# Kernel tuning notes

Hardware: AMD Instinct MI355X
Metric: run time of the kernel (lower is better)

Reference implementation:

```python
import jax, jax.numpy as jnp
import numpy as np

B, S, ENC = 64, 2048, 1024          # batch, encoder seq len, encoder feature dim
U, E_DIM, V_SZ = 512, 256, 50000    # dec_units, embedding_dim, vocab_size
IN_DIM = ENC + E_DIM                # LSTM input: [context ; token embedding]


def setup_inputs() -> dict:
    key = jax.random.key(0)
    ks = jax.random.split(key, 16)
    g = lambda k, shp, s=0.02: (jax.random.normal(k, shp, jnp.float32) * s)
    return {
        "x": jax.random.randint(ks[0], (B, 1), 0, V_SZ),
        "c_fwd": g(ks[1], (B, U), 0.1),
        "c_bwd": g(ks[2], (B, U), 0.1),
        "enc_output": jax.random.normal(ks[3], (B, S, ENC), jnp.float32),
        "emb": g(ks[4], (V_SZ, E_DIM)),
        "W1_w": g(ks[5], (ENC, U)), "W1_b": jnp.zeros((U,), jnp.float32),
        "W2_w": g(ks[6], (U, U)),   "W2_b": jnp.zeros((U,), jnp.float32),
        "W3_w": g(ks[7], (U, U)),   "W3_b": jnp.zeros((U,), jnp.float32),
        "V_w": g(ks[8], (U, 1)),    "V_b": jnp.zeros((1,), jnp.float32),
        "Kf": g(ks[9], (IN_DIM, 4 * U)),  "bf": jnp.zeros((4 * U,), jnp.float32),
        "Kb": g(ks[10], (IN_DIM, 4 * U)), "bb": jnp.zeros((4 * U,), jnp.float32),
        "fc_w": g(ks[11], (2 * U, V_SZ)), "fc_b": jnp.zeros((V_SZ,), jnp.float32),
    }


def _lstm_step_zero_state(xin, K, b):
    # Keras LSTM single step from zero (h0, c0): recurrent term vanishes.
    # Gate order in Keras kernel: i, f, c(g), o.
    z = xin @ K + b
    i, f, g, o = jnp.split(z, 4, axis=-1)
    i, o = jax.nn.sigmoid(i), jax.nn.sigmoid(o)  # f gate multiplies c0=0
    c = i * jnp.tanh(g)
    h = o * jnp.tanh(c)
    return h, c


def reference(x, c_fwd, c_bwd, enc_output, emb,
              W1_w, W1_b, W2_w, W2_b, W3_w, W3_b, V_w, V_b,
              Kf, bf, Kb, bb, fc_w, fc_b):
    # Bahdanau additive attention: score [B, S, 1]
    hidden_proj = (c_fwd @ W2_w + W2_b + c_bwd @ W3_w + W3_b)[:, None, :]  # [B,1,U]
    score = jnp.tanh(enc_output @ W1_w + W1_b + hidden_proj) @ V_w + V_b
    attn = jax.nn.softmax(score, axis=1)                 # softmax over S
    ctx = jnp.sum(attn * enc_output, axis=1)             # [B, ENC]

    xe = emb[x[:, 0]]                                    # [B, E_DIM]
    xin = jnp.concatenate([ctx, xe], axis=-1)            # [B, ENC+E_DIM]

    # Bidirectional LSTM over a length-1 sequence from zero initial state:
    # both directions see the same single timestep with separate weights.
    hf, cf = _lstm_step_zero_state(xin, Kf, bf)
    hb, cb = _lstm_step_zero_state(xin, Kb, bb)

    out = jnp.concatenate([hf, hb], axis=-1)             # [B, 2U]
    logits = out @ fc_w + fc_b                           # [B, vocab]
    return logits, hf, cf, hb, cb
```

## Files before the change

### kernel.cpp

```cpp
#include <hip/hip_runtime.h>

using u16 = unsigned short;
typedef float f32x4 __attribute__((ext_vector_type(4)));
typedef __bf16 bf16x8 __attribute__((ext_vector_type(8)));
typedef u16 u16x8 __attribute__((ext_vector_type(8)));
typedef u16 u16x4 __attribute__((ext_vector_type(4)));

static constexpr int OF_HPB   = 262144;
static constexpr int OF_CTXP  = 294912;
static constexpr int OF_STATS = 2392064;
static constexpr int OF_XIN   = 2394112;
static constexpr int OF_ZPART = 2476032;
static constexpr size_t SCRATCH_FLOATS = 3000320;
static constexpr size_t SCRATCH_BYTES  = SCRATCH_FLOATS * 4ull;
static constexpr size_t OF_W2P_F       = 3000320;
static constexpr size_t W2P_U16        = 50176ull * 1024ull;
static constexpr size_t TOTAL_BYTES    = OF_W2P_F * 4ull + W2P_U16 * 2ull;

#define FENCE()  asm volatile("" ::: "memory")
#define VMCNT6() asm volatile("s_waitcnt vmcnt(6)" ::: "memory")
#define VMCNT0() asm volatile("s_waitcnt vmcnt(0)" ::: "memory")
#define LGKM0()  asm volatile("s_waitcnt lgkmcnt(0)" ::: "memory")

__device__ __forceinline__ u16 f2bf(float f) {
  unsigned u = __float_as_uint(f);
  u += 0x7FFFu + ((u >> 16) & 1u);
  return (u16)(u >> 16);
}
__device__ __forceinline__ float bf2f(u16 u) {
  return __uint_as_float((unsigned)u << 16);
}
__device__ __forceinline__ float fast_tanh(float x) {
  x = fminf(fmaxf(x, -20.f), 20.f);
  float e = __expf(2.f * x);
  return (e - 1.f) / (e + 1.f);
}
__device__ __forceinline__ float fast_sig(float x) { return 1.f / (1.f + __expf(-x)); }

__device__ __forceinline__ void gll16(const u16* g, u16* l) {
  __builtin_amdgcn_global_load_lds(
      (const __attribute__((address_space(1))) unsigned int*)g,
      (__attribute__((address_space(3))) unsigned int*)l, 16, 0, 0);
}

__global__ void k_prep_w1(const float* __restrict__ W1w, u16* __restrict__ w1p) {
  __shared__ float tile[32][132];
  const int t = threadIdx.x;
  const int ks = blockIdx.x >> 2, u0 = (blockIdx.x & 3) * 128;
  {
    int kk = t >> 3, ui = (t & 7) * 16;
    const float* src = W1w + (size_t)(ks * 32 + kk) * 512 + u0 + ui;
    #pragma unroll
    for (int i = 0; i < 4; ++i)
      *(float4*)&tile[kk][ui + i * 4] = *(const float4*)(src + i * 4);
  }
  __syncthreads();
  {
    int u = t >> 1, kh = (t & 1) * 16;
    u16x8 p0, p1;
    #pragma unroll
    for (int i = 0; i < 8; ++i) {
      p0[i] = f2bf(tile[kh + i][u]);
      p1[i] = f2bf(tile[kh + 8 + i][u]);
    }
    u16* dst = w1p + ((size_t)ks * 512 + u0 + u) * 32 + kh;
    *(u16x8*)(dst)     = p0;
    *(u16x8*)(dst + 8) = p1;
  }
}

__global__ void k_prep_hp(const float* __restrict__ cf, const float* __restrict__ cb,
                          const float* __restrict__ W2w, const float* __restrict__ W2b,
                          const float* __restrict__ W3w, const float* __restrict__ W3b,
                          const float* __restrict__ W1b, float* __restrict__ hpb) {
  __shared__ float cfl[512], cbl[512];
  const int b = blockIdx.x, t = threadIdx.x;
  cfl[t] = cf[(size_t)b * 512 + t];       cfl[t + 256] = cf[(size_t)b * 512 + t + 256];
  cbl[t] = cb[(size_t)b * 512 + t];       cbl[t + 256] = cb[(size_t)b * 512 + t + 256];
  __syncthreads();
  const int u1 = t, u2 = t + 256;
  float a1 = W2b[u1] + W3b[u1] + W1b[u1];
  float a2 = W2b[u2] + W3b[u2] + W1b[u2];
  for (int k = 0; k < 512; ++k) {
    float c1 = cfl[k], c2 = cbl[k];
    const float* r2 = W2w + (size_t)k * 512;
    const float* r3 = W3w + (size_t)k * 512;
    a1 += c1 * r2[u1] + c2 * r3[u1];
    a2 += c1 * r2[u2] + c2 * r3[u2];
  }
  hpb[(size_t)b * 512 + u1] = a1;
  hpb[(size_t)b * 512 + u2] = a2;
}

__global__ void __launch_bounds__(256)
k_prep_fcw(const float* __restrict__ fcw, u16* __restrict__ w2p) {
  __shared__ float tl[32][260];
  const int t = threadIdx.x;
  const int jt = blockIdx.x >> 5, kt = blockIdx.x & 31;
  const int j0 = jt * 256, k0 = kt * 32;
  {
    const int kk = t >> 3, c0 = (t & 7) * 32;
    const float* src = fcw + (size_t)(k0 + kk) * 50000 + j0 + c0;
    #pragma unroll
    for (int i = 0; i < 8; ++i) {
      int j = j0 + c0 + i * 4;
      float4 v;
      if (j + 3 < 50000) {
        v = *(const float4*)(src + i * 4);
      } else {
        v.x = (j + 0 < 50000) ? src[i * 4 + 0] : 0.f;
        v.y = (j + 1 < 50000) ? src[i * 4 + 1] : 0.f;
        v.z = (j + 2 < 50000) ? src[i * 4 + 2] : 0.f;
        v.w = 0.f;
      }
      *(float4*)&tl[kk][c0 + i * 4] = v;
    }
  }
  __syncthreads();
  {
    u16* dst = w2p + ((size_t)kt * 50176 + j0 + t) * 32;
    #pragma unroll
    for (int q = 0; q < 4; ++q) {
      u16x8 p;
      #pragma unroll
      for (int m = 0; m < 8; ++m) p[m] = f2bf(tl[q * 8 + m][t]);
      *(u16x8*)(dst + q * 8) = p;
    }
  }
}

__global__ void __launch_bounds__(512, 4)
k_attn(const float* __restrict__ enc, const u16* __restrict__ w1p,
       const float* __restrict__ hpb, const float* __restrict__ Vw,
       const float* __restrict__ Vb, float* __restrict__ ctxp,
       float* __restrict__ stats) {
  __shared__ __align__(16) u16 smem[36864];

  const int t = threadIdx.x;
  const int bid = blockIdx.x;
  const int b = bid >> 5, tile = bid & 31;
  const size_t row0 = (size_t)b * 2048 + (size_t)tile * 64;

  const int l = t & 63, w = t >> 6;
  const int ln = l & 15, lg = l >> 4;

  const int s_im = t >> 7, s_ln = (t >> 3) & 15, s_lg = (t >> 1) & 3, s_h = t & 1;
  const float* a_src = enc + (row0 + s_im * 16 + s_ln) * 1024 + s_lg * 8 + s_h * 4;
  const int a_dst = (s_im * 64 + s_lg * 16 + s_ln) * 8 + s_h * 4;
  const u16* bsrc = w1p + (size_t)(w * 64 + ln) * 32 + lg * 8;
  u16* bdst = smem + w * 2048;

  f32x4 acc[4][4];
  #pragma unroll
  for (int im = 0; im < 4; ++im)
    #pragma unroll
    for (int nf = 0; nf < 4; ++nf) acc[im][nf] = f32x4{0.f, 0.f, 0.f, 0.f};

  float4 avH0, avH1, avH2;
  {
    float4 av0 = *(const float4*)(a_src);
    u16x4 aw;
    aw[0]=f2bf(av0.x); aw[1]=f2bf(av0.y); aw[2]=f2bf(av0.z); aw[3]=f2bf(av0.w);
    *(u16x4*)(smem + 32768 + a_dst) = aw;
    FENCE();
    avH0 = *(const float4*)(a_src + 32);
    avH1 = *(const float4*)(a_src + 64);
    FENCE();
    gll16(bsrc,        bdst);
    gll16(bsrc +  512, bdst +  512);
    gll16(bsrc + 1024, bdst + 1024);
    gll16(bsrc + 1536, bdst + 1536);
    FENCE();
    avH2 = *(const float4*)(a_src + 96);
    FENCE();
    LGKM0();
    __builtin_amdgcn_s_barrier();
  }

  #pragma unroll 4
  for (int ks = 0; ks < 28; ++ks) {
    const int cur = ks & 1;
    {
      u16* bd = bdst + ((cur ^ 1) << 14);
      const u16* bs = bsrc + (size_t)(ks + 1) * 16384;
      gll16(bs, bd);               gll16(bs +  512, bd +  512);
      gll16(bs + 1024, bd + 1024); gll16(bs + 1536, bd + 1536);
    }
    FENCE();
    float4 avIn = *(const float4*)(a_src + (ks + 4) * 32);
    FENCE();
    VMCNT6();
    const u16* Ac = smem + 32768 + (cur << 11);
    const u16* Bc = smem + (cur << 14) + w * 2048;
    bf16x8 afr[4], bfr[4];
    #pragma unroll
    for (int im = 0; im < 4; ++im) afr[im] = *(const bf16x8*)(Ac + im * 512 + l * 8);
    #pragma unroll
    for (int nf = 0; nf < 4; ++nf) bfr[nf] = *(const bf16x8*)(Bc + nf * 512 + l * 8);
    __builtin_amdgcn_s_setprio(1);
    #pragma unroll
    for (int im = 0; im < 4; ++im)
      #pragma unroll
      for (int nf = 0; nf < 4; ++nf)
        acc[im][nf] = __builtin_amdgcn_mfma_f32_16x16x32_bf16(afr[im], bfr[nf], acc[im][nf], 0, 0, 0);
    __builtin_amdgcn_s_setprio(0);
    {
      u16* An = smem + 32768 + ((cur ^ 1) << 11);
      u16x4 aw;
      aw[0]=f2bf(avH0.x); aw[1]=f2bf(avH0.y); aw[2]=f2bf(avH0.z); aw[3]=f2bf(avH0.w);
      *(u16x4*)(An + a_dst) = aw;
    }
    avH0 = avH1; avH1 = avH2; avH2 = avIn;
    LGKM0();
    __builtin_amdgcn_s_barrier();
  }

  for (int ks = 28; ks < 32; ++ks) {
    const int cur = ks & 1;
    if (ks < 31) {
      u16* bd = bdst + ((cur ^ 1) << 14);
      const u16* bs = bsrc + (size_t)(ks + 1) * 16384;
      gll16(bs, bd);               gll16(bs +  512, bd +  512);
      gll16(bs + 1024, bd + 1024); gll16(bs + 1536, bd + 1536);
    }
    VMCNT0();
    const u16* Ac = smem + 32768 + (cur << 11);
    const u16* Bc = smem + (cur << 14) + w * 2048;
    bf16x8 afr[4], bfr[4];
    #pragma unroll
    for (int im = 0; im < 4; ++im) afr[im] = *(const bf16x8*)(Ac + im * 512 + l * 8);
    #pragma unroll
    for (int nf = 0; nf < 4; ++nf) bfr[nf] = *(const bf16x8*)(Bc + nf * 512 + l * 8);
    #pragma unroll
    for (int im = 0; im < 4; ++im)
      #pragma unroll
      for (int nf = 0; nf < 4; ++nf)
        acc[im][nf] = __builtin_amdgcn_mfma_f32_16x16x32_bf16(afr[im], bfr[nf], acc[im][nf], 0, 0, 0);
    if (ks < 31) {
      u16* An = smem + 32768 + ((cur ^ 1) << 11);
      u16x4 aw;
      aw[0]=f2bf(avH0.x); aw[1]=f2bf(avH0.y); aw[2]=f2bf(avH0.z); aw[3]=f2bf(avH0.w);
      *(u16x4*)(An + a_dst) = aw;
      avH0 = avH1; avH1 = avH2;
    }
    LGKM0();
    __builtin_amdgcn_s_barrier();
  }

  float* fsm = (float*)smem;
  float* red = fsm;
  float* scv = fsm + 576;
  float* pcv = fsm + 640;

  float vw_l[4], hp_l[4];
  #pragma unroll
  for (int nf = 0; nf < 4; ++nf) {
    int col = w * 64 + nf * 16 + ln;
    vw_l[nf] = Vw[col];
    hp_l[nf] = hpb[(size_t)b * 512 + col];
  }
  #pragma unroll
  for (int im = 0; im < 4; ++im) {
    #pragma unroll
    for (int r = 0; r < 4; ++r) {
      float s = 0.f;
      #pragma unroll
      for (int nf = 0; nf < 4; ++nf)
        s += vw_l[nf] * fast_tanh(acc[im][nf][r] + hp_l[nf]);
      s += __shfl_xor(s, 1);
      s += __shfl_xor(s, 2);
      s += __shfl_xor(s, 4);
      s += __shfl_xor(s, 8);
      if (ln == 0) red[(im * 16 + lg * 4 + r) * 9 + w] = s;
    }
  }
  __syncthreads();
  if (t < 64) {
    float s = Vb[0];
    #pragma unroll
    for (int w2 = 0; w2 < 8; ++w2) s += red[t * 9 + w2];
    float e = __expf(s);
    scv[t] = e;
    float p = e;
    p += __shfl_xor(p, 1);  p += __shfl_xor(p, 2);  p += __shfl_xor(p, 4);
    p += __shfl_xor(p, 8);  p += __shfl_xor(p, 16); p += __shfl_xor(p, 32);
    if (t == 0) stats[bid] = p;
  }
  __syncthreads();

  {
    const int c4 = (t & 255) * 4;
    const int rh = t >> 8;
    const float* ep = enc + (row0 + rh * 32) * 1024 + c4;
    float ax = 0.f, ay = 0.f, az = 0.f, aw2 = 0.f;
    #pragma unroll 4
    for (int r = 0; r < 32; ++r) {
      float4 v = *(const float4*)(ep + (size_t)r * 1024);
      float s = scv[rh * 32 + r];
      ax += s * v.x; ay += s * v.y; az += s * v.z; aw2 += s * v.w;
    }
    if (t >= 256) {
      float4 st = {ax, ay, az, aw2};
      *(float4*)&pcv[c4] = st;
    }
    __syncthreads();
    if (t < 256) {
      float4 p2 = *(const float4*)&pcv[c4];
      float4 o = {ax + p2.x, ay + p2.y, az + p2.z, aw2 + p2.w};
      *(float4*)&ctxp[(size_t)bid * 1024 + c4] = o;
    }
  }
}

__global__ void k_attn_reduce(const float* __restrict__ ctxp, const float* __restrict__ stats,
                              const int* __restrict__ x, const float* __restrict__ emb,
                              float* __restrict__ xin) {
  __shared__ float ps[32];
  __shared__ float invs;
  const int b = blockIdx.x, t = threadIdx.x;
  if (t < 32) ps[t] = stats[b * 32 + t];
  __syncthreads();
  if (t == 0) {
    float s = 0.f;
    #pragma unroll
    for (int i = 0; i < 32; ++i) s += ps[i];
    invs = 1.f / s;
  }
  __syncthreads();
  const float inv = invs;
  #pragma unroll
  for (int i = 0; i < 4; ++i) {
    int c = t + i * 256;
    float a = 0.f;
    for (int chv = 0; chv < 32; ++chv)
      a += ctxp[((size_t)b * 32 + chv) * 1024 + c];
    xin[(size_t)b * 1280 + c] = a * inv;
  }
  xin[(size_t)b * 1280 + 1024 + t] = emb[(size_t)x[b] * 256 + t];
}

__global__ void k_lstm_gemm(const float* __restrict__ xin, const float* __restrict__ Kf,
                            const float* __restrict__ Kb, float* __restrict__ zpart) {
  __shared__ float xl[32][68];
  const int t = threadIdx.x;
  const int bid = blockIdx.x;
  const int dir = bid >> 7;
  const int jt  = (bid >> 1) & 63;
  const int ks  = bid & 1;
  const float* K = dir ? Kb : Kf;
  const int j  = jt * 32 + (t & 31);
  const int tb = t >> 5;
  const int brow = t >> 2, kq = (t & 3) * 8;
  float acc[8] = {0,0,0,0,0,0,0,0};
  for (int k0 = ks * 640; k0 < ks * 640 + 640; k0 += 32) {
    float4 x0 = *(const float4*)&xin[(size_t)brow * 1280 + k0 + kq];
    float4 x1 = *(const float4*)&xin[(size_t)brow * 1280 + k0 + kq + 4];
    __syncthreads();
    xl[kq+0][brow]=x0.x; xl[kq+1][brow]=x0.y; xl[kq+2][brow]=x0.z; xl[kq+3][brow]=x0.w;
    xl[kq+4][brow]=x1.x; xl[kq+5][brow]=x1.y; xl[kq+6][brow]=x1.z; xl[kq+7][brow]=x1.w;
    __syncthreads();
    const float* Kp = K + (size_t)k0 * 2048 + j;
    #pragma unroll 8
    for (int kk = 0; kk < 32; ++kk) {
      float wv = Kp[(size_t)kk * 2048];
      float4 v0 = *(const float4*)&xl[kk][tb * 8];
      float4 v1 = *(const float4*)&xl[kk][tb * 8 + 4];
      acc[0] += v0.x * wv; acc[1] += v0.y * wv; acc[2] += v0.z * wv; acc[3] += v0.w * wv;
      acc[4] += v1.x * wv; acc[5] += v1.y * wv; acc[6] += v1.z * wv; acc[7] += v1.w * wv;
    }
  }
  float* zp = zpart + ((size_t)dir * 2 + ks) * 64 * 2048;
  #pragma unroll
  for (int i = 0; i < 8; ++i)
    zp[(size_t)(tb * 8 + i) * 2048 + j] = acc[i];
}

__global__ void k_gates(const float* __restrict__ zpart, const float* __restrict__ bfv,
                        const float* __restrict__ bbv, float* __restrict__ dout) {
  const int dir = blockIdx.x >> 6, b = blockIdx.x & 63, u = threadIdx.x;
  const float* bias = dir ? bbv : bfv;
  const float* z0 = zpart + ((size_t)dir * 2 + 0) * 131072 + (size_t)b * 2048;
  const float* z1 = zpart + ((size_t)dir * 2 + 1) * 131072 + (size_t)b * 2048;
  float zi = z0[u]        + z1[u]        + bias[u];
  float zg = z0[1024 + u] + z1[1024 + u] + bias[1024 + u];
  float zo = z0[1536 + u] + z1[1536 + u] + bias[1536 + u];
  float c = fast_sig(zi) * fast_tanh(zg);
  float h = fast_sig(zo) * fast_tanh(c);
  size_t base = 3200000u + (size_t)dir * 65536u;
  dout[base + (size_t)b * 512 + u] = h;
  dout[base + 32768u + (size_t)b * 512 + u] = c;
}

__global__ void __launch_bounds__(256)
k_fc_mfma(const float* __restrict__ hbase, const u16* __restrict__ w2p,
          const float* __restrict__ fcb, float* __restrict__ logits) {
  __shared__ __align__(16) u16 smem[24576];
  const int t = threadIdx.x;
  const int j0 = blockIdx.x * 256;
  const int l = t & 63, w = t >> 6;
  const int ln = l & 15, lg = l >> 4;

  const int s_im = t >> 6, s_ln = (t >> 2) & 15, s_lg = t & 3;
  const int a_chunk = (s_im * 64 + s_lg * 16 + s_ln) * 8;
  const int a_row = s_im * 16 + s_ln;

  const u16* bsrc = w2p + (size_t)(j0 + w * 64 + ln) * 32 + lg * 8;
  u16* bdst = smem + w * 2048;

  f32x4 acc[4][4];
  #pragma unroll
  for (int im = 0; im < 4; ++im)
    #pragma unroll
    for (int nf = 0; nf < 4; ++nf) acc[im][nf] = f32x4{0.f, 0.f, 0.f, 0.f};

  {
    gll16(bsrc,        bdst);
    gll16(bsrc +  512, bdst +  512);
    gll16(bsrc + 1024, bdst + 1024);
    gll16(bsrc + 1536, bdst + 1536);
    const float* hs = hbase + (size_t)a_row * 512 + s_lg * 8;
    float4 v0 = *(const float4*)(hs);
    float4 v1 = *(const float4*)(hs + 4);
    float vv[8] = {v0.x, v0.y, v0.z, v0.w, v1.x, v1.y, v1.z, v1.w};
    u16x8 hi, lo;
    #pragma unroll
    for (int jq = 0; jq < 8; ++jq) {
      u16 h = f2bf(vv[jq]);
      hi[jq] = h;
      lo[jq] = f2bf(vv[jq] - bf2f(h));
    }
    *(u16x8*)(smem + 16384 + a_chunk) = hi;
    *(u16x8*)(smem + 16384 + 2048 + a_chunk) = lo;
  }
  __syncthreads();

  for (int ks = 0; ks < 32; ++ks) {
    const int cur = ks & 1;
    if (ks < 31) {
      u16* bd = bdst + ((cur ^ 1) << 13);
      const u16* bs = bsrc + (size_t)(ks + 1) * 1605632;
      gll16(bs, bd);               gll16(bs +  512, bd +  512);
      gll16(bs + 1024, bd + 1024); gll16(bs + 1536, bd + 1536);
    }
    const u16* Ac = smem + 16384 + (cur << 12);
    const u16* Bc = smem + (cur << 13) + w * 2048;
    bf16x8 ahi[4], alo[4], bfr[4];
    #pragma unroll
    for (int im = 0; im < 4; ++im) {
      ahi[im] = *(const bf16x8*)(Ac + im * 512 + l * 8);
      alo[im] = *(const bf16x8*)(Ac + 2048 + im * 512 + l * 8);
    }
    #pragma unroll
    for (int nf = 0; nf < 4; ++nf) bfr[nf] = *(const bf16x8*)(Bc + nf * 512 + l * 8);
    #pragma unroll
    for (int im = 0; im < 4; ++im)
      #pragma unroll
      for (int nf = 0; nf < 4; ++nf) {
        acc[im][nf] = __builtin_amdgcn_mfma_f32_16x16x32_bf16(alo[im], bfr[nf], acc[im][nf], 0, 0, 0);
        acc[im][nf] = __builtin_amdgcn_mfma_f32_16x16x32_bf16(ahi[im], bfr[nf], acc[im][nf], 0, 0, 0);
      }
    if (ks < 31) {
      const int kn = ks + 1;
      const float* hs = hbase + (kn >= 16 ? 65536 : 0) + (size_t)a_row * 512 + (kn & 15) * 32 + s_lg * 8;
      float4 v0 = *(const float4*)(hs);
      float4 v1 = *(const float4*)(hs + 4);
      float vv[8] = {v0.x, v0.y, v0.z, v0.w, v1.x, v1.y, v1.z, v1.w};
      u16x8 hi, lo;
      #pragma unroll
      for (int jq = 0; jq < 8; ++jq) {
        u16 h = f2bf(vv[jq]);
        hi[jq] = h;
        lo[jq] = f2bf(vv[jq] - bf2f(h));
      }
      u16* An = smem + 16384 + ((cur ^ 1) << 12);
      *(u16x8*)(An + a_chunk) = hi;
      *(u16x8*)(An + 2048 + a_chunk) = lo;
    }
    __syncthreads();
  }

  float fb[4];
  #pragma unroll
  for (int nf = 0; nf < 4; ++nf) {
    int c = j0 + w * 64 + nf * 16 + ln;
    fb[nf] = (c < 50000) ? fcb[c] : 0.f;
  }
  #pragma unroll
  for (int im = 0; im < 4; ++im)
    #pragma unroll
    for (int nf = 0; nf < 4; ++nf) {
      int c = j0 + w * 64 + nf * 16 + ln;
      if (c < 50000) {
        #pragma unroll
        for (int r = 0; r < 4; ++r) {
          int row = im * 16 + lg * 4 + r;
          logits[(size_t)row * 50000 + c] = acc[im][nf][r] + fb[nf];
        }
      }
    }
}

__global__ void __launch_bounds__(256)
k_fc_f32(const float* __restrict__ dout_ro, const float* __restrict__ fcw,
         const float* __restrict__ fcb, float* __restrict__ logits) {
  __shared__ float ol[64][68];
  __shared__ float wl[64][132];
  const int t = threadIdx.x;
  const int j0 = blockIdx.x * 128;
  const int tb = t >> 5, tj = t & 31;
  const float* hf = dout_ro + 3200000u;
  const float* hb = dout_ro + 3200000u + 65536u;
  float acc[8][4];
  #pragma unroll
  for (int bi = 0; bi < 8; ++bi)
    #pragma unroll
    for (int ji = 0; ji < 4; ++ji) acc[bi][ji] = 0.f;

  for (int k0 = 0; k0 < 1024; k0 += 64) {
    __syncthreads();
    {
      int bb = t >> 2, kq = (t & 3) * 16;
      const float* src = (k0 < 512) ? (hf + (size_t)bb * 512 + k0 + kq)
                                    : (hb + (size_t)bb * 512 + (k0 - 512) + kq);
      #pragma unroll
      for (int i = 0; i < 4; ++i) {
        float4 v = *(const float4*)(src + i * 4);
        ol[kq + i*4 + 0][bb] = v.x;
        ol[kq + i*4 + 1][bb] = v.y;
        ol[kq + i*4 + 2][bb] = v.z;
        ol[kq + i*4 + 3][bb] = v.w;
      }
    }
    {
      int kk = t >> 2, jh = (t & 3) * 32;
      const float* wsrc = fcw + (size_t)(k0 + kk) * 50000 + j0 + jh;
      #pragma unroll
      for (int i = 0; i < 8; ++i) {
        int j = j0 + jh + i * 4;
        float4 v;
        if (j + 3 < 50000) {
          v = *(const float4*)(wsrc + i * 4);
        } else {
          v.x = (j + 0 < 50000) ? wsrc[i*4 + 0] : 0.f;
          v.y = (j + 1 < 50000) ? wsrc[i*4 + 1] : 0.f;
          v.z = (j + 2 < 50000) ? wsrc[i*4 + 2] : 0.f;
          v.w = 0.f;
        }
        *(float4*)&wl[kk][jh + i * 4] = v;
      }
    }
    __syncthreads();
    #pragma unroll 4
    for (int kk = 0; kk < 64; ++kk) {
      float4 wv = *(const float4*)&wl[kk][tj * 4];
      float4 q0 = *(const float4*)&ol[kk][tb * 8];
      float4 q1 = *(const float4*)&ol[kk][tb * 8 + 4];
      float obv[8] = {q0.x, q0.y, q0.z, q0.w, q1.x, q1.y, q1.z, q1.w};
      #pragma unroll
      for (int bi = 0; bi < 8; ++bi) {
        acc[bi][0] += obv[bi] * wv.x;
        acc[bi][1] += obv[bi] * wv.y;
        acc[bi][2] += obv[bi] * wv.z;
        acc[bi][3] += obv[bi] * wv.w;
      }
    }
  }

  const int j = j0 + tj * 4;
  if (j + 3 < 50000) {
    float4 fb = *(const float4*)(fcb + j);
    #pragma unroll
    for (int bi = 0; bi < 8; ++bi) {
      float4 r;
      r.x = acc[bi][0] + fb.x; r.y = acc[bi][1] + fb.y;
      r.z = acc[bi][2] + fb.z; r.w = acc[bi][3] + fb.w;
      *(float4*)&logits[(size_t)(tb * 8 + bi) * 50000 + j] = r;
    }
  } else {
    for (int ji = 0; ji < 4; ++ji) {
      if (j + ji < 50000) {
        float fb = fcb[j + ji];
        for (int bi = 0; bi < 8; ++bi)
          logits[(size_t)(tb * 8 + bi) * 50000 + j + ji] = acc[bi][ji] + fb;
      }
    }
  }
}

extern "C" void kernel_launch(void* const* d_in, const int* in_sizes, int n_in,
                              void* d_out, int out_size, void* d_ws, size_t ws_size,
                              hipStream_t stream) {
  const int*   x    = (const int*)  d_in[0];
  const float* cfwd = (const float*)d_in[1];
  const float* cbwd = (const float*)d_in[2];
  const float* enc  = (const float*)d_in[3];
  const float* emb  = (const float*)d_in[4];
  const float* W1w  = (const float*)d_in[5];
  const float* W1b  = (const float*)d_in[6];
  const float* W2w  = (const float*)d_in[7];
  const float* W2b  = (const float*)d_in[8];
  const float* W3w  = (const float*)d_in[9];
  const float* W3b  = (const float*)d_in[10];
  const float* Vw   = (const float*)d_in[11];
  const float* Vb   = (const float*)d_in[12];
  const float* Kf   = (const float*)d_in[13];
  const float* bfv  = (const float*)d_in[14];
  const float* Kb   = (const float*)d_in[15];
  const float* bbv  = (const float*)d_in[16];
  const float* fcw  = (const float*)d_in[17];
  const float* fcb  = (const float*)d_in[18];
  float* out = (float*)d_out;

  const bool haveWs  = (ws_size >= SCRATCH_BYTES);
  const bool bigWs   = (ws_size >= TOTAL_BYTES);
  float* S = haveWs ? (float*)d_ws : out;
  u16*   w1p   = (u16*)S;
  float* hpb   = S + OF_HPB;
  float* ctxp  = S + OF_CTXP;
  float* stats = S + OF_STATS;
  float* xin   = S + OF_XIN;
  float* zpart = S + OF_ZPART;
  u16*   w2p   = (u16*)(S + OF_W2P_F);

  k_prep_w1<<<128, 256, 0, stream>>>(W1w, w1p);
  k_prep_hp<<<64, 256, 0, stream>>>(cfwd, cbwd, W2w, W2b, W3w, W3b, W1b, hpb);
  if (bigWs) k_prep_fcw<<<6272, 256, 0, stream>>>(fcw, w2p);
  k_attn<<<2048, 512, 0, stream>>>(enc, w1p, hpb, Vw, Vb, ctxp, stats);
  k_attn_reduce<<<64, 256, 0, stream>>>(ctxp, stats, x, emb, xin);
  k_lstm_gemm<<<256, 256, 0, stream>>>(xin, Kf, Kb, zpart);
  k_gates<<<128, 512, 0, stream>>>(zpart, bfv, bbv, out);
  if (bigWs) k_fc_mfma<<<196, 256, 0, stream>>>(out + 3200000u, w2p, fcb, out);
  else       k_fc_f32<<<391, 256, 0, stream>>>(out, fcw, fcb, out);
}
```

Before: 591.1 us.

## Split attention into score and context kernels, simplify pipeline, halve FC tile width

The fused attention kernel, which computed scores and per-tile partial contexts, becomes a score-only kernel plus a separate k_ctx kernel. k_ctx does the softmax and the weighted sum over the sequence, which drops the partial-context scratch and its reduction pass. The score kernel's hand-tuned prefetch pipeline (raw waitcnt asm, setprio, three-deep A prefetch) is replaced by a simpler loop that prefetches one tile ahead and syncs with __syncthreads. The FC MFMA kernel's tile narrows from 256 to 128 columns, doubling the grid to 392 blocks. Cost: k_ctx reads enc_output (512 MB) a second time, and the A-operand prefetch is shallower.

```diff
diff --git a/kernel.cpp b/kernel.cpp
--- a/kernel.cpp
+++ b/kernel.cpp
@@ -7,20 +7,14 @@
 typedef u16 u16x4 __attribute__((ext_vector_type(4)));
 
 static constexpr int OF_HPB   = 262144;
-static constexpr int OF_CTXP  = 294912;
-static constexpr int OF_STATS = 2392064;
-static constexpr int OF_XIN   = 2394112;
-static constexpr int OF_ZPART = 2476032;
-static constexpr size_t SCRATCH_FLOATS = 3000320;
+static constexpr int OF_SCORE = 294912;
+static constexpr int OF_XIN   = 425984;
+static constexpr int OF_ZPART = 507904;
+static constexpr size_t SCRATCH_FLOATS = 1032192;
 static constexpr size_t SCRATCH_BYTES  = SCRATCH_FLOATS * 4ull;
-static constexpr size_t OF_W2P_F       = 3000320;
+static constexpr size_t OF_W2P_F       = 1032192;
 static constexpr size_t W2P_U16        = 50176ull * 1024ull;
 static constexpr size_t TOTAL_BYTES    = OF_W2P_F * 4ull + W2P_U16 * 2ull;
-
-#define FENCE()  asm volatile("" ::: "memory")
-#define VMCNT6() asm volatile("s_waitcnt vmcnt(6)" ::: "memory")
-#define VMCNT0() asm volatile("s_waitcnt vmcnt(0)" ::: "memory")
-#define LGKM0()  asm volatile("s_waitcnt lgkmcnt(0)" ::: "memory")
 
 __device__ __forceinline__ u16 f2bf(float f) {
   unsigned u = __float_as_uint(f);
@@ -130,10 +124,9 @@
 }
 
 __global__ void __launch_bounds__(512, 4)
-k_attn(const float* __restrict__ enc, const u16* __restrict__ w1p,
-       const float* __restrict__ hpb, const float* __restrict__ Vw,
-       const float* __restrict__ Vb, float* __restrict__ ctxp,
-       float* __restrict__ stats) {
+k_score(const float* __restrict__ enc, const u16* __restrict__ w1p,
+        const float* __restrict__ hpb, const float* __restrict__ Vw,
+        const float* __restrict__ Vb, float* __restrict__ score) {
   __shared__ __align__(16) u16 smem[36864];
 
   const int t = threadIdx.x;
@@ -156,40 +149,33 @@
     #pragma unroll
     for (int nf = 0; nf < 4; ++nf) acc[im][nf] = f32x4{0.f, 0.f, 0.f, 0.f};
 
-  float4 avH0, avH1, avH2;
+  float4 avB;
   {
     float4 av0 = *(const float4*)(a_src);
     u16x4 aw;
     aw[0]=f2bf(av0.x); aw[1]=f2bf(av0.y); aw[2]=f2bf(av0.z); aw[3]=f2bf(av0.w);
     *(u16x4*)(smem + 32768 + a_dst) = aw;
-    FENCE();
-    avH0 = *(const float4*)(a_src + 32);
-    avH1 = *(const float4*)(a_src + 64);
-    FENCE();
     gll16(bsrc,        bdst);
     gll16(bsrc +  512, bdst +  512);
     gll16(bsrc + 1024, bdst + 1024);
     gll16(bsrc + 1536, bdst + 1536);
-    FENCE();
-    avH2 = *(const float4*)(a_src + 96);
-    FENCE();
-    LGKM0();
-    __builtin_amdgcn_s_barrier();
-  }
-
-  #pragma unroll 4
-  for (int ks = 0; ks < 28; ++ks) {
+    avB = *(const float4*)(a_src + 32);
+  }
+  __syncthreads();
+
+  for (int ks = 0; ks < 32; ++ks) {
     const int cur = ks & 1;
-    {
+    if (ks < 31) {
+      u16* An = smem + 32768 + ((cur ^ 1) << 11);
+      u16x4 aw;
+      aw[0]=f2bf(avB.x); aw[1]=f2bf(avB.y); aw[2]=f2bf(avB.z); aw[3]=f2bf(avB.w);
+      *(u16x4*)(An + a_dst) = aw;
+      if (ks < 30) avB = *(const float4*)(a_src + (ks + 2) * 32);
       u16* bd = bdst + ((cur ^ 1) << 14);
       const u16* bs = bsrc + (size_t)(ks + 1) * 16384;
       gll16(bs, bd);               gll16(bs +  512, bd +  512);
       gll16(bs + 1024, bd + 1024); gll16(bs + 1536, bd + 1536);
     }
-    FENCE();
-    float4 avIn = *(const float4*)(a_src + (ks + 4) * 32);
-    FENCE();
-    VMCNT6();
     const u16* Ac = smem + 32768 + (cur << 11);
     const u16* Bc = smem + (cur << 14) + w * 2048;
     bf16x8 afr[4], bfr[4];
@@ -197,60 +183,16 @@
     for (int im = 0; im < 4; ++im) afr[im] = *(const bf16x8*)(Ac + im * 512 + l * 8);
     #pragma unroll
     for (int nf = 0; nf < 4; ++nf) bfr[nf] = *(const bf16x8*)(Bc + nf * 512 + l * 8);
-    __builtin_amdgcn_s_setprio(1);
     #pragma unroll
     for (int im = 0; im < 4; ++im)
       #pragma unroll
       for (int nf = 0; nf < 4; ++nf)
         acc[im][nf] = __builtin_amdgcn_mfma_f32_16x16x32_bf16(afr[im], bfr[nf], acc[im][nf], 0, 0, 0);
-    __builtin_amdgcn_s_setprio(0);
-    {
-      u16* An = smem + 32768 + ((cur ^ 1) << 11);
-      u16x4 aw;
-      aw[0]=f2bf(avH0.x); aw[1]=f2bf(avH0.y); aw[2]=f2bf(avH0.z); aw[3]=f2bf(avH0.w);
-      *(u16x4*)(An + a_dst) = aw;
-    }
-    avH0 = avH1; avH1 = avH2; avH2 = avIn;
-    LGKM0();
-    __builtin_amdgcn_s_barrier();
-  }
-
-  for (int ks = 28; ks < 32; ++ks) {
-    const int cur = ks & 1;
-    if (ks < 31) {
-      u16* bd = bdst + ((cur ^ 1) << 14);
-      const u16* bs = bsrc + (size_t)(ks + 1) * 16384;
-      gll16(bs, bd);               gll16(bs +  512, bd +  512);
-      gll16(bs + 1024, bd + 1024); gll16(bs + 1536, bd + 1536);
-    }
-    VMCNT0();
-    const u16* Ac = smem + 32768 + (cur << 11);
-    const u16* Bc = smem + (cur << 14) + w * 2048;
-    bf16x8 afr[4], bfr[4];
-    #pragma unroll
-    for (int im = 0; im < 4; ++im) afr[im] = *(const bf16x8*)(Ac + im * 512 + l * 8);
-    #pragma unroll
-    for (int nf = 0; nf < 4; ++nf) bfr[nf] = *(const bf16x8*)(Bc + nf * 512 + l * 8);
-    #pragma unroll
-    for (int im = 0; im < 4; ++im)
-      #pragma unroll
-      for (int nf = 0; nf < 4; ++nf)
-        acc[im][nf] = __builtin_amdgcn_mfma_f32_16x16x32_bf16(afr[im], bfr[nf], acc[im][nf], 0, 0, 0);
-    if (ks < 31) {
-      u16* An = smem + 32768 + ((cur ^ 1) << 11);
-      u16x4 aw;
-      aw[0]=f2bf(avH0.x); aw[1]=f2bf(avH0.y); aw[2]=f2bf(avH0.z); aw[3]=f2bf(avH0.w);
-      *(u16x4*)(An + a_dst) = aw;
-      avH0 = avH1; avH1 = avH2;
-    }
-    LGKM0();
-    __builtin_amdgcn_s_barrier();
+    __syncthreads();
   }
 
   float* fsm = (float*)smem;
   float* red = fsm;
-  float* scv = fsm + 576;
-  float* pcv = fsm + 640;
 
   float vw_l[4], hp_l[4];
   #pragma unroll
@@ -279,63 +221,53 @@
     float s = Vb[0];
     #pragma unroll
     for (int w2 = 0; w2 < 8; ++w2) s += red[t * 9 + w2];
-    float e = __expf(s);
-    scv[t] = e;
-    float p = e;
-    p += __shfl_xor(p, 1);  p += __shfl_xor(p, 2);  p += __shfl_xor(p, 4);
-    p += __shfl_xor(p, 8);  p += __shfl_xor(p, 16); p += __shfl_xor(p, 32);
-    if (t == 0) stats[bid] = p;
-  }
-  __syncthreads();
-
-  {
-    const int c4 = (t & 255) * 4;
-    const int rh = t >> 8;
-    const float* ep = enc + (row0 + rh * 32) * 1024 + c4;
-    float ax = 0.f, ay = 0.f, az = 0.f, aw2 = 0.f;
-    #pragma unroll 4
-    for (int r = 0; r < 32; ++r) {
-      float4 v = *(const float4*)(ep + (size_t)r * 1024);
-      float s = scv[rh * 32 + r];
-      ax += s * v.x; ay += s * v.y; az += s * v.z; aw2 += s * v.w;
-    }
-    if (t >= 256) {
-      float4 st = {ax, ay, az, aw2};
-      *(float4*)&pcv[c4] = st;
-    }
-    __syncthreads();
-    if (t < 256) {
-      float4 p2 = *(const float4*)&pcv[c4];
-      float4 o = {ax + p2.x, ay + p2.y, az + p2.z, aw2 + p2.w};
-      *(float4*)&ctxp[(size_t)bid * 1024 + c4] = o;
-    }
-  }
-}
-
-__global__ void k_attn_reduce(const float* __restrict__ ctxp, const float* __restrict__ stats,
-                              const int* __restrict__ x, const float* __restrict__ emb,
-                              float* __restrict__ xin) {
-  __shared__ float ps[32];
-  __shared__ float invs;
+    score[row0 + t] = s;
+  }
+}
+
+__global__ void k_ctx(const float* __restrict__ enc, const float* __restrict__ score,
+                      float* __restrict__ xin) {
+  __shared__ float esm[2048];
+  __shared__ float reds[256];
+  const int t = threadIdx.x;
+  const int b = blockIdx.x >> 3, ct = blockIdx.x & 7;
+  float p = 0.f;
+  for (int s = t; s < 2048; s += 256) {
+    float e = __expf(score[(size_t)b * 2048 + s]);
+    esm[s] = e;
+    p += e;
+  }
+  reds[t] = p;
+  __syncthreads();
+  for (int off = 128; off > 0; off >>= 1) {
+    if (t < off) reds[t] += reds[t + off];
+    __syncthreads();
+  }
+  const float inv = 1.f / reds[0];
+  __syncthreads();
+  const int c = ct * 128 + (t & 127);
+  const int sp = t >> 7;
+  const float* ep = enc + (size_t)b * 2048 * 1024 + c;
+  float a0=0,a1=0,a2=0,a3=0,a4=0,a5=0,a6=0,a7=0;
+  for (int s = sp; s < 2048; s += 16) {
+    a0 += esm[s+ 0] * ep[(size_t)(s+ 0) * 1024];
+    a1 += esm[s+ 2] * ep[(size_t)(s+ 2) * 1024];
+    a2 += esm[s+ 4] * ep[(size_t)(s+ 4) * 1024];
+    a3 += esm[s+ 6] * ep[(size_t)(s+ 6) * 1024];
+    a4 += esm[s+ 8] * ep[(size_t)(s+ 8) * 1024];
+    a5 += esm[s+10] * ep[(size_t)(s+10) * 1024];
+    a6 += esm[s+12] * ep[(size_t)(s+12) * 1024];
+    a7 += esm[s+14] * ep[(size_t)(s+14) * 1024];
+  }
+  float a = ((a0+a1)+(a2+a3)) + ((a4+a5)+(a6+a7));
+  reds[t] = a;
+  __syncthreads();
+  if (t < 128) xin[(size_t)b * 1280 + c] = (reds[t] + reds[t + 128]) * inv;
+}
+
+__global__ void k_xe(const int* __restrict__ x, const float* __restrict__ emb,
+                     float* __restrict__ xin) {
   const int b = blockIdx.x, t = threadIdx.x;
-  if (t < 32) ps[t] = stats[b * 32 + t];
-  __syncthreads();
-  if (t == 0) {
-    float s = 0.f;
-    #pragma unroll
-    for (int i = 0; i < 32; ++i) s += ps[i];
-    invs = 1.f / s;
-  }
-  __syncthreads();
-  const float inv = invs;
-  #pragma unroll
-  for (int i = 0; i < 4; ++i) {
-    int c = t + i * 256;
-    float a = 0.f;
-    for (int chv = 0; chv < 32; ++chv)
-      a += ctxp[((size_t)b * 32 + chv) * 1024 + c];
-    xin[(size_t)b * 1280 + c] = a * inv;
-  }
   xin[(size_t)b * 1280 + 1024 + t] = emb[(size_t)x[b] * 256 + t];
 }
 
@@ -394,9 +326,9 @@
 __global__ void __launch_bounds__(256)
 k_fc_mfma(const float* __restrict__ hbase, const u16* __restrict__ w2p,
           const float* __restrict__ fcb, float* __restrict__ logits) {
-  __shared__ __align__(16) u16 smem[24576];
-  const int t = threadIdx.x;
-  const int j0 = blockIdx.x * 256;
+  __shared__ __align__(16) u16 smem[16384];
+  const int t = threadIdx.x;
+  const int j0 = blockIdx.x * 128;
   const int l = t & 63, w = t >> 6;
   const int ln = l & 15, lg = l >> 4;
 
@@ -404,20 +336,18 @@
   const int a_chunk = (s_im * 64 + s_lg * 16 + s_ln) * 8;
   const int a_row = s_im * 16 + s_ln;
 
-  const u16* bsrc = w2p + (size_t)(j0 + w * 64 + ln) * 32 + lg * 8;
-  u16* bdst = smem + w * 2048;
-
-  f32x4 acc[4][4];
+  const u16* bsrc = w2p + (size_t)(j0 + w * 32 + ln) * 32 + lg * 8;
+  u16* bdst = smem + w * 1024;
+
+  f32x4 acc[4][2];
   #pragma unroll
   for (int im = 0; im < 4; ++im)
     #pragma unroll
-    for (int nf = 0; nf < 4; ++nf) acc[im][nf] = f32x4{0.f, 0.f, 0.f, 0.f};
+    for (int nf = 0; nf < 2; ++nf) acc[im][nf] = f32x4{0.f, 0.f, 0.f, 0.f};
 
   {
-    gll16(bsrc,        bdst);
-    gll16(bsrc +  512, bdst +  512);
-    gll16(bsrc + 1024, bdst + 1024);
-    gll16(bsrc + 1536, bdst + 1536);
+    gll16(bsrc,       bdst);
+    gll16(bsrc + 512, bdst + 512);
     const float* hs = hbase + (size_t)a_row * 512 + s_lg * 8;
     float4 v0 = *(const float4*)(hs);
     float4 v1 = *(const float4*)(hs + 4);
@@ -429,37 +359,18 @@
       hi[jq] = h;
       lo[jq] = f2bf(vv[jq] - bf2f(h));
     }
-    *(u16x8*)(smem + 16384 + a_chunk) = hi;
-    *(u16x8*)(smem + 16384 + 2048 + a_chunk) = lo;
+    *(u16x8*)(smem + 8192 + a_chunk) = hi;
+    *(u16x8*)(smem + 8192 + 2048 + a_chunk) = lo;
   }
   __syncthreads();
 
   for (int ks = 0; ks < 32; ++ks) {
     const int cur = ks & 1;
     if (ks < 31) {
-      u16* bd = bdst + ((cur ^ 1) << 13);
+      u16* bd = smem + ((cur ^ 1) << 12) + w * 1024;
       const u16* bs = bsrc + (size_t)(ks + 1) * 1605632;
-      gll16(bs, bd);               gll16(bs +  512, bd +  512);
-      gll16(bs + 1024, bd + 1024); gll16(bs + 1536, bd + 1536);
-    }
-    const u16* Ac = smem + 16384 + (cur << 12);
-    const u16* Bc = smem + (cur << 13) + w * 2048;
-    bf16x8 ahi[4], alo[4], bfr[4];
-    #pragma unroll
-    for (int im = 0; im < 4; ++im) {
-      ahi[im] = *(const bf16x8*)(Ac + im * 512 + l * 8);
-      alo[im] = *(const bf16x8*)(Ac + 2048 + im * 512 + l * 8);
-    }
-    #pragma unroll
-    for (int nf = 0; nf < 4; ++nf) bfr[nf] = *(const bf16x8*)(Bc + nf * 512 + l * 8);
-    #pragma unroll
-    for (int im = 0; im < 4; ++im)
-      #pragma unroll
-      for (int nf = 0; nf < 4; ++nf) {
-        acc[im][nf] = __builtin_amdgcn_mfma_f32_16x16x32_bf16(alo[im], bfr[nf], acc[im][nf], 0, 0, 0);
-        acc[im][nf] = __builtin_amdgcn_mfma_f32_16x16x32_bf16(ahi[im], bfr[nf], acc[im][nf], 0, 0, 0);
-      }
-    if (ks < 31) {
+      gll16(bs, bd);
+      gll16(bs + 512, bd + 512);
       const int kn = ks + 1;
       const float* hs = hbase + (kn >= 16 ? 65536 : 0) + (size_t)a_row * 512 + (kn & 15) * 32 + s_lg * 8;
       float4 v0 = *(const float4*)(hs);
@@ -472,32 +383,44 @@
         hi[jq] = h;
         lo[jq] = f2bf(vv[jq] - bf2f(h));
       }
-      u16* An = smem + 16384 + ((cur ^ 1) << 12);
+      u16* An = smem + 8192 + ((cur ^ 1) << 12);
       *(u16x8*)(An + a_chunk) = hi;
       *(u16x8*)(An + 2048 + a_chunk) = lo;
     }
-    __syncthreads();
-  }
-
-  float fb[4];
-  #pragma unroll
-  for (int nf = 0; nf < 4; ++nf) {
-    int c = j0 + w * 64 + nf * 16 + ln;
-    fb[nf] = (c < 50000) ? fcb[c] : 0.f;
-  }
-  #pragma unroll
-  for (int im = 0; im < 4; ++im)
-    #pragma unroll
-    for (int nf = 0; nf < 4; ++nf) {
-      int c = j0 + w * 64 + nf * 16 + ln;
-      if (c < 50000) {
+    const u16* Ac = smem + 8192 + (cur << 12);
+    const u16* Bc = smem + (cur << 12) + w * 1024;
+    bf16x8 ahi[4], alo[4], bfr[2];
+    #pragma unroll
+    for (int im = 0; im < 4; ++im) {
+      ahi[im] = *(const bf16x8*)(Ac + im * 512 + l * 8);
+      alo[im] = *(const bf16x8*)(Ac + 2048 + im * 512 + l * 8);
+    }
+    #pragma unroll
+    for (int nf = 0; nf < 2; ++nf) bfr[nf] = *(const bf16x8*)(Bc + nf * 512 + l * 8);
+    #pragma unroll
+    for (int im = 0; im < 4; ++im)
+      #pragma unroll
+      for (int nf = 0; nf < 2; ++nf) {
+        acc[im][nf] = __builtin_amdgcn_mfma_f32_16x16x32_bf16(alo[im], bfr[nf], acc[im][nf], 0, 0, 0);
+        acc[im][nf] = __builtin_amdgcn_mfma_f32_16x16x32_bf16(ahi[im], bfr[nf], acc[im][nf], 0, 0, 0);
+      }
+    __syncthreads();
+  }
+
+  #pragma unroll
+  for (int nf = 0; nf < 2; ++nf) {
+    int c = j0 + w * 32 + nf * 16 + ln;
+    if (c < 50000) {
+      float fb = fcb[c];
+      #pragma unroll
+      for (int im = 0; im < 4; ++im)
         #pragma unroll
         for (int r = 0; r < 4; ++r) {
           int row = im * 16 + lg * 4 + r;
-          logits[(size_t)row * 50000 + c] = acc[im][nf][r] + fb[nf];
+          logits[(size_t)row * 50000 + c] = acc[im][nf][r] + fb;
         }
-      }
-    }
+    }
+  }
 }
 
 __global__ void __launch_bounds__(256)
@@ -611,13 +534,12 @@
   const float* fcb  = (const float*)d_in[18];
   float* out = (float*)d_out;
 
-  const bool haveWs  = (ws_size >= SCRATCH_BYTES);
-  const bool bigWs   = (ws_size >= TOTAL_BYTES);
+  const bool haveWs = (ws_size >= SCRATCH_BYTES);
+  const bool bigWs  = (ws_size >= TOTAL_BYTES);
   float* S = haveWs ? (float*)d_ws : out;
   u16*   w1p   = (u16*)S;
   float* hpb   = S + OF_HPB;
-  float* ctxp  = S + OF_CTXP;
-  float* stats = S + OF_STATS;
+  float* score = S + OF_SCORE;
   float* xin   = S + OF_XIN;
   float* zpart = S + OF_ZPART;
   u16*   w2p   = (u16*)(S + OF_W2P_F);
@@ -625,10 +547,11 @@
   k_prep_w1<<<128, 256, 0, stream>>>(W1w, w1p);
   k_prep_hp<<<64, 256, 0, stream>>>(cfwd, cbwd, W2w, W2b, W3w, W3b, W1b, hpb);
   if (bigWs) k_prep_fcw<<<6272, 256, 0, stream>>>(fcw, w2p);
-  k_attn<<<2048, 512, 0, stream>>>(enc, w1p, hpb, Vw, Vb, ctxp, stats);
-  k_attn_reduce<<<64, 256, 0, stream>>>(ctxp, stats, x, emb, xin);
+  k_score<<<2048, 512, 0, stream>>>(enc, w1p, hpb, Vw, Vb, score);
+  k_ctx<<<512, 256, 0, stream>>>(enc, score, xin);
+  k_xe<<<64, 256, 0, stream>>>(x, emb, xin);
   k_lstm_gemm<<<256, 256, 0, stream>>>(xin, Kf, Kb, zpart);
   k_gates<<<128, 512, 0, stream>>>(zpart, bfv, bbv, out);
-  if (bigWs) k_fc_mfma<<<196, 256, 0, stream>>>(out + 3200000u, w2p, fcb, out);
+  if (bigWs) k_fc_mfma<<<392, 256, 0, stream>>>(out + 3200000u, w2p, fcb, out);
   else       k_fc_f32<<<391, 256, 0, stream>>>(out, fcw, fcb, out);
 }
```

After: 617.4 us. 1.04x slower.
